# Optimization experiments

Measured on AMD Instinct MI355X. Metric: run time of the kernel, lower is better.

The kernel has to match this reference:

```python
import jax, jax.numpy as jnp
import numpy as np

D_MODEL = 1024
N_HEAD = 16
D_HEAD = D_MODEL // N_HEAD
N_EXPERTS = 8
TOP_K = 2
D_FF = 4096
EPS = 1e-6


def setup_inputs() -> dict:
    key = jax.random.key(0)
    ks = jax.random.split(key, 16)
    s = 0.02  # init scale
    d, dff, E = D_MODEL, D_FF, N_EXPERTS
    return {
        "dec": jax.random.normal(ks[0], (4, 1024, d), jnp.float32),
        "text_encoder": jax.random.normal(ks[1], (4, 512, d), jnp.float32),
        # self-attention projections
        "Wq1": jax.random.normal(ks[2], (d, d), jnp.float32) * s,
        "Wk1": jax.random.normal(ks[3], (d, d), jnp.float32) * s,
        "Wv1": jax.random.normal(ks[4], (d, d), jnp.float32) * s,
        "Wo1": jax.random.normal(ks[5], (d, d), jnp.float32) * s,
        # cross-attention projections
        "Wq2": jax.random.normal(ks[6], (d, d), jnp.float32) * s,
        "Wk2": jax.random.normal(ks[7], (d, d), jnp.float32) * s,
        "Wv2": jax.random.normal(ks[8], (d, d), jnp.float32) * s,
        "Wo2": jax.random.normal(ks[9], (d, d), jnp.float32) * s,
        # shared RMSNorm gain (module uses one norm instance three times)
        "g": jnp.ones((d,), jnp.float32),
        # MoE router + per-expert FFN weights
        "Wg": jax.random.normal(ks[10], (d, E), jnp.float32) * s,
        "W1": jax.random.normal(ks[11], (E, d, dff), jnp.float32) * s,
        "W2": jax.random.normal(ks[12], (E, dff, d), jnp.float32) * s,
    }


def rmsnorm(x, g):
    return x * jax.lax.rsqrt(jnp.mean(x * x, axis=-1, keepdims=True) + EPS) * g


def mha(q_in, k_in, v_in, Wq, Wk, Wv, Wo):
    B, Sq, _ = q_in.shape
    Sk = k_in.shape[1]
    q = (q_in @ Wq).reshape(B, Sq, N_HEAD, D_HEAD)
    k = (k_in @ Wk).reshape(B, Sk, N_HEAD, D_HEAD)
    v = (v_in @ Wv).reshape(B, Sk, N_HEAD, D_HEAD)
    scores = jnp.einsum("bqhd,bkhd->bhqk", q, k) / jnp.sqrt(jnp.asarray(D_HEAD, q.dtype))
    attn = jax.nn.softmax(scores, axis=-1)
    out = jnp.einsum("bhqk,bkhd->bqhd", attn, v).reshape(B, Sq, D_MODEL)
    return out @ Wo


def moe(x, Wg, W1, W2):
    # top-k softmax router, renormalized weights; dense per-expert FFN with combine
    probs = jax.nn.softmax(x @ Wg, axis=-1)              # [B,S,E]
    weights, indices = jax.lax.top_k(probs, TOP_K)        # [B,S,k]
    weights = weights / jnp.sum(weights, axis=-1, keepdims=True)
    # combine[t,e] = sum_k weights[t,k] * (indices[t,k]==e)
    combine = jnp.sum(
        jax.nn.one_hot(indices, N_EXPERTS, dtype=x.dtype) * weights[..., None], axis=-2
    )  # [B,S,E]
    out = jnp.zeros_like(x)
    for e in range(N_EXPERTS):  # fixed small expert loop
        h = jax.nn.relu(x @ W1[e]) @ W2[e]
        out = out + combine[..., e:e + 1] * h
    return weights, indices, out


def reference(dec, text_encoder, Wq1, Wk1, Wv1, Wo1, Wq2, Wk2, Wv2, Wo2, g, Wg, W1, W2):
    # self-attention + residual + RMSNorm (dropout p=0 -> identity)
    x = rmsnorm(mha(dec, dec, dec, Wq1, Wk1, Wv1, Wo1) + dec, g)
    # cross-attention + residual + RMSNorm
    x = rmsnorm(mha(x, text_encoder, text_encoder, Wq2, Wk2, Wv2, Wo2) + x, g)
    # MoE FFN + residual + RMSNorm
    weights, indices, y = moe(x, Wg, W1, W2)
    x = rmsnorm(y + x, g)
    return weights, indices, x
```

## Files before the change

### kernel.cpp

```cpp
#include <hip/hip_runtime.h>
#include <stdint.h>

#define D_    1024
#define BB    4
#define SDEC  1024
#define STXT  512
#define TDEC  4096
#define TTXT  2048
#define NH    16
#define DHD   64
#define NE    8
#define DFF   4096
#define NSLOT 8192
#define ND1   8192
#define ND2   4096
#define MOEGRID 1024

using u16 = unsigned short;
typedef __attribute__((ext_vector_type(8))) short bf16x8;
typedef __attribute__((ext_vector_type(4))) float f32x4;

__device__ __forceinline__ float bf2f(u16 h) {
    union { unsigned int u; float f; } x; x.u = ((unsigned int)h) << 16; return x.f;
}
__device__ __forceinline__ u16 f2bf(float f) {
    union { float f; unsigned int u; } x; x.f = f;
    unsigned int lsb = (x.u >> 16) & 1u;
    return (u16)((x.u + 0x7fffu + lsb) >> 16);
}

__device__ __forceinline__ void gld16(const u16* g, u16* l) {
    __builtin_amdgcn_global_load_lds((const __attribute__((address_space(1))) void*)g,
                                     (__attribute__((address_space(3))) void*)l,
                                     16, 0, 0);
}

constexpr int BM = 128, BK = 32;

template<int SPLIT, int EPI, int BROWS>
__global__ __launch_bounds__(256) void gemm_bt(
    const u16* __restrict__ AH, const u16* __restrict__ AL,
    const u16* __restrict__ BH, const u16* __restrict__ BL,
    float* __restrict__ Cf, u16* __restrict__ CH, u16* __restrict__ CL,
    int M, int N, int K, int lda, int ldb, int ldc,
    long strA, long strB, long strC)
{
    constexpr int WM = (BROWS == 64) ? 2 : 4;
    constexpr int ASZ = BM * BK, BSZ = BROWS * BK;
    __shared__ u16 smem[(SPLIT ? 2 : 1) * (ASZ + BSZ)];
    u16* sAH = smem;
    u16* sBH = smem + ASZ;
    u16* sAL = SPLIT ? smem + ASZ + BSZ : nullptr;
    u16* sBL = SPLIT ? smem + 2 * ASZ + BSZ : nullptr;

    const int z = blockIdx.z;
    const long zA = (long)z * strA, zB = (long)z * strB, zC = (long)z * strC;

    const int tileM = blockIdx.y * BM, tileN = blockIdx.x * BROWS;
    const int t = threadIdx.x;
    const int sr = t >> 2;
    const int sc = (t & 3) << 3;
    const u16* pA = AH + zA + (long)(tileM + sr) * lda + sc;
    const u16* pB = BH + zB + (long)(tileN + sr) * ldb + sc;
    const u16* pAl = nullptr; const u16* pBl = nullptr;
    if constexpr (SPLIT) {
        pAl = AL + zA + (long)(tileM + sr) * lda + sc;
        pBl = BL + zB + (long)(tileN + sr) * ldb + sc;
    }
    const long hA = 64L * lda, hB = 64L * ldb;

    const int lane = t & 63;
    const int wv = t >> 6;
    const int wr = (BROWS == 64) ? (wv << 5) : ((wv >> 1) << 6);
    const int wc = (BROWS == 64) ? 0 : ((wv & 1) << 6);
    const int fr = lane & 15, kg = lane >> 4;

    f32x4 acc[WM][4];
    const f32x4 vzero = {0.f, 0.f, 0.f, 0.f};
#pragma unroll
    for (int m = 0; m < WM; ++m)
#pragma unroll
        for (int n = 0; n < 4; ++n) acc[m][n] = vzero;

    for (int k0 = 0; k0 < K; k0 += BK) {
        gld16(pA + k0,      sAH + t * 8);
        gld16(pA + k0 + hA, sAH + 2048 + t * 8);
        gld16(pB + k0,      sBH + t * 8);
        if constexpr (BROWS == 128) gld16(pB + k0 + hB, sBH + 2048 + t * 8);
        if constexpr (SPLIT) {
            gld16(pAl + k0,      sAL + t * 8);
            gld16(pAl + k0 + hA, sAL + 2048 + t * 8);
            gld16(pBl + k0,      sBL + t * 8);
            if constexpr (BROWS == 128) gld16(pBl + k0 + hB, sBL + 2048 + t * 8);
        }
        __syncthreads();

        bf16x8 fa[WM], fb[4], fal[WM], fbl[4];
#pragma unroll
        for (int m = 0; m < WM; ++m) {
            fa[m] = *(const bf16x8*)&sAH[(wr + m * 16 + fr) * BK + (kg << 3)];
            if constexpr (SPLIT) fal[m] = *(const bf16x8*)&sAL[(wr + m * 16 + fr) * BK + (kg << 3)];
        }
#pragma unroll
        for (int n = 0; n < 4; ++n) {
            fb[n] = *(const bf16x8*)&sBH[(wc + n * 16 + fr) * BK + (kg << 3)];
            if constexpr (SPLIT) fbl[n] = *(const bf16x8*)&sBL[(wc + n * 16 + fr) * BK + (kg << 3)];
        }
#pragma unroll
        for (int m = 0; m < WM; ++m)
#pragma unroll
            for (int n = 0; n < 4; ++n) {
                acc[m][n] = __builtin_amdgcn_mfma_f32_16x16x32_bf16(fa[m], fb[n], acc[m][n], 0, 0, 0);
                if constexpr (SPLIT) {
                    acc[m][n] = __builtin_amdgcn_mfma_f32_16x16x32_bf16(fa[m],  fbl[n], acc[m][n], 0, 0, 0);
                    acc[m][n] = __builtin_amdgcn_mfma_f32_16x16x32_bf16(fal[m], fb[n],  acc[m][n], 0, 0, 0);
                }
            }
        __syncthreads();
    }

#pragma unroll
    for (int m = 0; m < WM; ++m) {
        const int r0 = tileM + wr + m * 16 + (kg << 2);
#pragma unroll
        for (int n = 0; n < 4; ++n) {
            const int col = tileN + wc + n * 16 + fr;
            if (col >= N) continue;
#pragma unroll
            for (int i = 0; i < 4; ++i) {
                const int r = r0 + i;
                if (r >= M) continue;
                const float v = acc[m][n][i];
                const long off = zC + (long)r * ldc + col;
                if constexpr (EPI == 0) {
                    Cf[off] = v;
                } else if constexpr (EPI == 1) {
                    const u16 h = f2bf(v);
                    CH[off] = h;
                    CL[off] = f2bf(v - bf2f(h));
                } else {
                    CH[off] = f2bf(fmaxf(v, 0.f));
                }
            }
        }
    }
}

template<int EPI>
__global__ __launch_bounds__(256, 4) void moe_gemm2(
    const u16* __restrict__ Ag, int lda,
    const u16* __restrict__ BTbase, int ldb, long btStride,
    float* __restrict__ Cf0, float* __restrict__ Cf1, u16* __restrict__ CH, int ldc,
    const int4* __restrict__ desc, int ndesc, int Kiter)
{
    __shared__ u16 smem[16384];
    const int t = threadIdx.x;
    const int lane = t & 63, wv = t >> 6;
    const int wr = (wv >> 1) << 6, wc = (wv & 1) << 6;
    const int fr = lane & 15, kg = lane >> 4;
    const int nks = Kiter >> 5;

    const int rS = t >> 2;
    const int cS = ((t & 3) ^ ((t >> 3) & 3)) << 3;

    int ldsA[4], ldsB[4];
#pragma unroll
    for (int m = 0; m < 4; ++m) {
        const int ra = wr + m * 16 + fr;
        ldsA[m] = ra * 32 + ((kg ^ ((ra >> 1) & 3)) << 3);
        const int rb = wc + m * 16 + fr;
        ldsB[m] = rb * 32 + ((kg ^ ((rb >> 1) & 3)) << 3);
    }

    for (int p = blockIdx.x; p < ndesc; p += MOEGRID) {
        const int4 d = desc[p];
        if (d.x < 0) continue;
        const int rowbase = d.x, colbase = d.y & 0xFFFF, e = d.y >> 16;
        const int kbase = d.z, s1 = d.w;
        const u16* paS = Ag + (long)(rowbase + rS) * lda + kbase + cS;
        const u16* pbS = BTbase + (long)e * btStride + (long)(colbase + rS) * ldb + kbase + cS;
        const long hA = 64L * lda, hB = 64L * ldb;

        f32x4 acc[4][4];
        const f32x4 vzero = {0.f, 0.f, 0.f, 0.f};
#pragma unroll
        for (int m = 0; m < 4; ++m)
#pragma unroll
            for (int n = 0; n < 4; ++n) acc[m][n] = vzero;

#define STG(ks, buf) { const long k0_ = (long)(ks) << 5; \
        u16* sA_ = smem + (buf) * 8192; \
        gld16(paS + k0_,      sA_ + t * 8); \
        gld16(paS + k0_ + hA, sA_ + 2048 + t * 8); \
        gld16(pbS + k0_,      sA_ + 4096 + t * 8); \
        gld16(pbS + k0_ + hB, sA_ + 6144 + t * 8); }

        STG(0, 0);
        asm volatile("s_waitcnt vmcnt(0)" ::: "memory");
        __builtin_amdgcn_s_barrier();

        for (int ks = 0; ks < nks; ++ks) {
            const int cur = ks & 1;
            if (ks + 1 < nks) STG(ks + 1, cur ^ 1);
            const u16* sA = smem + cur * 8192;
            const u16* sB = sA + 4096;
            bf16x8 fa[4], fb[4];
#pragma unroll
            for (int m = 0; m < 4; ++m) fa[m] = *(const bf16x8*)&sA[ldsA[m]];
#pragma unroll
            for (int n = 0; n < 4; ++n) fb[n] = *(const bf16x8*)&sB[ldsB[n]];
#pragma unroll
            for (int m = 0; m < 4; ++m)
#pragma unroll
                for (int n = 0; n < 4; ++n)
                    acc[m][n] = __builtin_amdgcn_mfma_f32_16x16x32_bf16(fa[m], fb[n], acc[m][n], 0, 0, 0);
            asm volatile("s_waitcnt vmcnt(0)" ::: "memory");
            __builtin_amdgcn_s_barrier();
        }
#undef STG

        float* __restrict__ C = (EPI == 0) ? ((kbase == 0) ? Cf0 : Cf1) : nullptr;
#pragma unroll
        for (int m = 0; m < 4; ++m) {
            const int r0 = rowbase + wr + m * 16 + (kg << 2);
#pragma unroll
            for (int n = 0; n < 4; ++n) {
                const int col = colbase + wc + n * 16 + fr;
#pragma unroll
                for (int i = 0; i < 4; ++i) {
                    const int r = r0 + i;
                    if (r >= s1) continue;
                    const float v = acc[m][n][i];
                    const long off = (long)r * ldc + col;
                    if constexpr (EPI == 0) C[off] = v;
                    else                    CH[off] = f2bf(fmaxf(v, 0.f));
                }
            }
        }
    }
}

__global__ __launch_bounds__(256) void split2k(const float* __restrict__ in,
                                               u16* __restrict__ oh, u16* __restrict__ ol, long n)
{
    long i = ((long)blockIdx.x * 256 + threadIdx.x) * 4;
    if (i >= n) return;
    float4 v = *(const float4*)(in + i);
    u16 h0 = f2bf(v.x), h1 = f2bf(v.y), h2 = f2bf(v.z), h3 = f2bf(v.w);
    uint2 oo;
    oo.x = (unsigned)h0 | ((unsigned)h1 << 16);
    oo.y = (unsigned)h2 | ((unsigned)h3 << 16);
    *(uint2*)(oh + i) = oo;
    if (ol) {
        u16 l0 = f2bf(v.x - bf2f(h0)), l1 = f2bf(v.y - bf2f(h1));
        u16 l2 = f2bf(v.z - bf2f(h2)), l3 = f2bf(v.w - bf2f(h3));
        uint2 ll;
        ll.x = (unsigned)l0 | ((unsigned)l1 << 16);
        ll.y = (unsigned)l2 | ((unsigned)l3 << 16);
        *(uint2*)(ol + i) = ll;
    }
}

__global__ __launch_bounds__(256) void transpose_split(
    const float* __restrict__ in, u16* __restrict__ oh, u16* __restrict__ ol,
    int R, int C, int ild, long ibs1, long ibs2, int nb2, int old_, long obs)
{
    __shared__ float tile[32][33];
    const int z = blockIdx.z;
    const float* ip = in + (long)(z / nb2) * ibs1 + (long)(z % nb2) * ibs2;
    u16* ohp = oh + (long)z * obs;
    u16* olp = ol ? ol + (long)z * obs : nullptr;
    const int c0 = blockIdx.x * 32, r0 = blockIdx.y * 32;
    const int tx = threadIdx.x & 31, ty = threadIdx.x >> 5;
    for (int i = ty; i < 32; i += 8) {
        int r = r0 + i, c = c0 + tx;
        tile[i][tx] = (r < R && c < C) ? ip[(long)r * ild + c] : 0.f;
    }
    __syncthreads();
    for (int i = ty; i < 32; i += 8) {
        int oc = c0 + i, orr = r0 + tx;
        if (oc < C && orr < R) {
            float v = tile[tx][i];
            u16 h = f2bf(v);
            ohp[(long)oc * old_ + orr] = h;
            if (olp) olp[(long)oc * old_ + orr] = f2bf(v - bf2f(h));
        }
    }
}

__global__ __launch_bounds__(256) void transpose_split_hl(
    const u16* __restrict__ inH, const u16* __restrict__ inL,
    u16* __restrict__ oh, u16* __restrict__ ol,
    int R, int C, int ild, long ibs1, long ibs2, int nb2, int old_, long obs)
{
    __shared__ float tile[32][33];
    const int z = blockIdx.z;
    const long base = (long)(z / nb2) * ibs1 + (long)(z % nb2) * ibs2;
    u16* ohp = oh + (long)z * obs;
    u16* olp = ol + (long)z * obs;
    const int c0 = blockIdx.x * 32, r0 = blockIdx.y * 32;
    const int tx = threadIdx.x & 31, ty = threadIdx.x >> 5;
    for (int i = ty; i < 32; i += 8) {
        int r = r0 + i, c = c0 + tx;
        float v = 0.f;
        if (r < R && c < C) {
            const long o = base + (long)r * ild + c;
            v = bf2f(inH[o]) + bf2f(inL[o]);
        }
        tile[i][tx] = v;
    }
    __syncthreads();
    for (int i = ty; i < 32; i += 8) {
        int oc = c0 + i, orr = r0 + tx;
        if (oc < C && orr < R) {
            float v = tile[tx][i];
            u16 h = f2bf(v);
            ohp[(long)oc * old_ + orr] = h;
            olp[(long)oc * old_ + orr] = f2bf(v - bf2f(h));
        }
    }
}

__global__ __launch_bounds__(256) void softmax_split(
    const float* __restrict__ s, u16* __restrict__ ph, u16* __restrict__ pl,
    int cols, float scale)
{
    const float* p = s + (long)blockIdx.x * cols;
    u16* php = ph + (long)blockIdx.x * cols;
    u16* plp = pl + (long)blockIdx.x * cols;
    const int t = threadIdx.x;
    float v[4];
    int vpt;
    if (cols == 1024) {
        vpt = 4;
        float4 x = ((const float4*)p)[t];
        v[0] = x.x * scale; v[1] = x.y * scale; v[2] = x.z * scale; v[3] = x.w * scale;
    } else {
        vpt = 2;
        float2 x = ((const float2*)p)[t];
        v[0] = x.x * scale; v[1] = x.y * scale; v[2] = -3.4e38f; v[3] = -3.4e38f;
    }
    float mx = fmaxf(fmaxf(v[0], v[1]), fmaxf(v[2], v[3]));
#pragma unroll
    for (int o = 32; o; o >>= 1) mx = fmaxf(mx, __shfl_xor(mx, o));
    __shared__ float sm[4];
    const int wv = t >> 6, ln = t & 63;
    if (ln == 0) sm[wv] = mx;
    __syncthreads();
    mx = fmaxf(fmaxf(sm[0], sm[1]), fmaxf(sm[2], sm[3]));
    float sum = 0.f;
    for (int i = 0; i < vpt; ++i) { v[i] = expf(v[i] - mx); sum += v[i]; }
#pragma unroll
    for (int o = 32; o; o >>= 1) sum += __shfl_xor(sum, o);
    __shared__ float ss[4];
    if (ln == 0) ss[wv] = sum;
    __syncthreads();
    sum = ss[0] + ss[1] + ss[2] + ss[3];
    const float inv = 1.f / sum;
    if (cols == 1024) {
        float q0 = v[0] * inv, q1 = v[1] * inv, q2 = v[2] * inv, q3 = v[3] * inv;
        u16 h0 = f2bf(q0), h1 = f2bf(q1), h2 = f2bf(q2), h3 = f2bf(q3);
        uint2 hh; hh.x = (unsigned)h0 | ((unsigned)h1 << 16); hh.y = (unsigned)h2 | ((unsigned)h3 << 16);
        ((uint2*)php)[t] = hh;
        u16 l0 = f2bf(q0 - bf2f(h0)), l1 = f2bf(q1 - bf2f(h1));
        u16 l2 = f2bf(q2 - bf2f(h2)), l3 = f2bf(q3 - bf2f(h3));
        uint2 ll; ll.x = (unsigned)l0 | ((unsigned)l1 << 16); ll.y = (unsigned)l2 | ((unsigned)l3 << 16);
        ((uint2*)plp)[t] = ll;
    } else {
        float q0 = v[0] * inv, q1 = v[1] * inv;
        u16 h0 = f2bf(q0), h1 = f2bf(q1);
        ((unsigned*)php)[t] = (unsigned)h0 | ((unsigned)h1 << 16);
        u16 l0 = f2bf(q0 - bf2f(h0)), l1 = f2bf(q1 - bf2f(h1));
        ((unsigned*)plp)[t] = (unsigned)l0 | ((unsigned)l1 << 16);
    }
}

__global__ __launch_bounds__(256) void add_rmsnorm(
    const float* __restrict__ a, const float* __restrict__ b, const float* __restrict__ g,
    float* __restrict__ xo, u16* __restrict__ xh, u16* __restrict__ xl)
{
    const long row = blockIdx.x;
    const int t = threadIdx.x;
    const float* pa = a + row * D_;
    const float* pb = b + row * D_;
    float v[4]; double ssq = 0.0;
#pragma unroll
    for (int i = 0; i < 4; ++i) {
        int c = t + (i << 8);
        v[i] = pa[c] + pb[c];
        ssq += (double)v[i] * v[i];
    }
#pragma unroll
    for (int o = 32; o; o >>= 1) ssq += __shfl_xor(ssq, o);
    __shared__ double sd[4];
    if ((t & 63) == 0) sd[t >> 6] = ssq;
    __syncthreads();
    ssq = sd[0] + sd[1] + sd[2] + sd[3];
    const float rs = (float)(1.0 / sqrt(ssq * (1.0 / 1024.0) + 1e-6));
#pragma unroll
    for (int i = 0; i < 4; ++i) {
        int c = t + (i << 8);
        float o = v[i] * rs * g[c];
        xo[row * D_ + c] = o;
        if (xh) {
            u16 h = f2bf(o);
            xh[row * D_ + c] = h;
            if (xl) xl[row * D_ + c] = f2bf(o - bf2f(h));
        }
    }
}

__global__ __launch_bounds__(256) void router_topk(
    const float* __restrict__ x2, const float* __restrict__ Wg,
    float* __restrict__ outw, float* __restrict__ outi,
    int* __restrict__ idx, float* __restrict__ tokw, int* __restrict__ counts, int T)
{
    const int wid = (int)((blockIdx.x * 256 + threadIdx.x) >> 6);
    const int lane = threadIdx.x & 63;
    if (wid >= T) return;
    float acc[NE];
#pragma unroll
    for (int e = 0; e < NE; ++e) acc[e] = 0.f;
    const float* xr = x2 + (long)wid * D_;
    for (int i = 0; i < 16; ++i) {
        float xv = xr[i * 64 + lane];
        const float* wr = Wg + (long)(i * 64 + lane) * NE;
#pragma unroll
        for (int e = 0; e < NE; ++e) acc[e] += xv * wr[e];
    }
#pragma unroll
    for (int e = 0; e < NE; ++e)
#pragma unroll
        for (int o = 32; o; o >>= 1) acc[e] += __shfl_xor(acc[e], o);
    if (lane == 0) {
        float m = acc[0];
#pragma unroll
        for (int e = 1; e < NE; ++e) m = fmaxf(m, acc[e]);
        float p[NE], s = 0.f;
#pragma unroll
        for (int e = 0; e < NE; ++e) { p[e] = expf(acc[e] - m); s += p[e]; }
        const float invs = 1.f / s;
#pragma unroll
        for (int e = 0; e < NE; ++e) p[e] *= invs;
        int e0 = 0;
#pragma unroll
        for (int e = 1; e < NE; ++e) if (p[e] > p[e0]) e0 = e;
        int e1 = (e0 == 0) ? 1 : 0;
#pragma unroll
        for (int e = 0; e < NE; ++e) if (e != e0 && e != e1 && p[e] > p[e1]) e1 = e;
        float w0 = p[e0], w1 = p[e1];
        const float sw = 1.f / (w0 + w1);
        w0 *= sw; w1 *= sw;
        outw[2 * wid] = w0;      outw[2 * wid + 1] = w1;
        outi[2 * wid] = (float)e0; outi[2 * wid + 1] = (float)e1;
        idx[2 * wid] = e0;       idx[2 * wid + 1] = e1;
        tokw[2 * wid] = w0;      tokw[2 * wid + 1] = w1;
        atomicAdd(&counts[e0], 1);
        atomicAdd(&counts[e1], 1);
    }
}

__global__ void scan_desc(const int* __restrict__ counts, int* __restrict__ cursor,
                          int4* __restrict__ d1, int4* __restrict__ d2)
{
    __shared__ int sseg[NE + 1];
    if (threadIdx.x == 0) {
        int a = 0;
        for (int e = 0; e < NE; ++e) { sseg[e] = a; cursor[e] = a; a += counts[e]; }
        sseg[NE] = a;
    }
    __syncthreads();
    const int e = threadIdx.x;
    if (e < NE) {
        const int s0 = sseg[e], s1 = sseg[e + 1];
        const int nyt = (s1 - s0 + 127) >> 7;
        for (int xt = 0; xt < 32; ++xt)
            for (int yt = 0; yt < nyt; ++yt)
                d1[e + 8 * (xt * nyt + yt)] =
                    make_int4(s0 + yt * 128, (xt * 128) | (e << 16), 0, s1);
        for (int kh = 0; kh < 2; ++kh)
            for (int xt = 0; xt < 8; ++xt)
                for (int yt = 0; yt < nyt; ++yt)
                    d2[e + 8 * ((kh * 8 + xt) * nyt + yt)] =
                        make_int4(s0 + yt * 128, (xt * 128) | (e << 16), kh * 2048, s1);
    }
}

__global__ __launch_bounds__(256) void scatter_slots(
    const int* __restrict__ idx, int* __restrict__ cursor,
    int* __restrict__ row_token, int* __restrict__ slot_of, int T)
{
    const int t = blockIdx.x * 256 + threadIdx.x;
    if (t >= T) return;
#pragma unroll
    for (int k = 0; k < 2; ++k) {
        const int e = idx[2 * t + k];
        const int pos = atomicAdd(&cursor[e], 1);
        row_token[pos] = t;
        slot_of[2 * t + k] = pos;
    }
}

__global__ __launch_bounds__(256) void gather_bf16(
    const float* __restrict__ x2, const int* __restrict__ row_token, u16* __restrict__ Xg)
{
    const int r = blockIdx.x;
    const int t = threadIdx.x;
    const float* src = x2 + (long)row_token[r] * D_ + t * 4;
    float4 v = *(const float4*)src;
    uint2 oo;
    oo.x = (unsigned)f2bf(v.x) | ((unsigned)f2bf(v.y) << 16);
    oo.y = (unsigned)f2bf(v.z) | ((unsigned)f2bf(v.w) << 16);
    *(uint2*)(Xg + (long)r * D_ + t * 4) = oo;
}

__global__ __launch_bounds__(256) void combine_rmsnorm(
    const float* __restrict__ Y0, const float* __restrict__ Y1,
    const int* __restrict__ slot_of, const float* __restrict__ tokw,
    const float* __restrict__ x2, const float* __restrict__ g, float* __restrict__ out)
{
    const long tr = blockIdx.x;
    const int t = threadIdx.x;
    const int s0 = slot_of[2 * tr], s1 = slot_of[2 * tr + 1];
    const float w0 = tokw[2 * tr], w1 = tokw[2 * tr + 1];
    const float* ya0 = Y0 + (long)s0 * D_;
    const float* yb0 = Y1 + (long)s0 * D_;
    const float* ya1 = Y0 + (long)s1 * D_;
    const float* yb1 = Y1 + (long)s1 * D_;
    const float* xr = x2 + tr * D_;
    float v[4]; double ssq = 0.0;
#pragma unroll
    for (int i = 0; i < 4; ++i) {
        int c = t + (i << 8);
        v[i] = w0 * (ya0[c] + yb0[c]) + w1 * (ya1[c] + yb1[c]) + xr[c];
        ssq += (double)v[i] * v[i];
    }
#pragma unroll
    for (int o = 32; o; o >>= 1) ssq += __shfl_xor(ssq, o);
    __shared__ double sd[4];
    if ((t & 63) == 0) sd[t >> 6] = ssq;
    __syncthreads();
    ssq = sd[0] + sd[1] + sd[2] + sd[3];
    const float rs = (float)(1.0 / sqrt(ssq * (1.0 / 1024.0) + 1e-6));
#pragma unroll
    for (int i = 0; i < 4; ++i) {
        int c = t + (i << 8);
        out[tr * D_ + c] = v[i] * rs * g[c];
    }
}

__global__ void sentinel(float* o) { o[0] = 12345.0f; }

extern "C" void kernel_launch(void* const* d_in, const int* in_sizes, int n_in,
                              void* d_out, int out_size, void* d_ws, size_t ws_size,
                              hipStream_t stream)
{
    const float* dec = (const float*)d_in[0];
    const float* te  = (const float*)d_in[1];
    const float* Win[8] = { (const float*)d_in[2], (const float*)d_in[3], (const float*)d_in[4],
                            (const float*)d_in[5], (const float*)d_in[6], (const float*)d_in[7],
                            (const float*)d_in[8], (const float*)d_in[9] };
    const float* g  = (const float*)d_in[10];
    const float* Wg = (const float*)d_in[11];
    const float* W1 = (const float*)d_in[12];
    const float* W2 = (const float*)d_in[13];
    float* outw = (float*)d_out;
    float* outi = outw + 2 * TDEC;
    float* outx = outw + 4 * TDEC;

    char* ws = (char*)d_ws;
    size_t off = 0;
    auto A = [&](size_t bytes) -> char* {
        char* p = ws + off;
        off += (bytes + 255) & ~(size_t)255;
        return p;
    };

    u16* decH = (u16*)A((size_t)TDEC * D_ * 2);
    u16* decL = (u16*)A((size_t)TDEC * D_ * 2);
    u16* teH  = (u16*)A((size_t)TTXT * D_ * 2);
    u16* teL  = (u16*)A((size_t)TTXT * D_ * 2);
    u16* wtHall = (u16*)A((size_t)8 * D_ * D_ * 2);
    u16* wtLall = (u16*)A((size_t)8 * D_ * D_ * 2);
    float* x1f = (float*)A((size_t)TDEC * D_ * 4);
    float* x2f = (float*)A((size_t)TDEC * D_ * 4);
    float* tokw = (float*)A(NSLOT * 4);
    int* idx    = (int*)A(NSLOT * 4);
    int* counts = (int*)A(256);
    int* cursor = (int*)A(256);
    int* row_token = (int*)A(NSLOT * 4);
    int* slot_of   = (int*)A(NSLOT * 4);
    int4* desc1 = (int4*)A((size_t)ND1 * 16);
    int4* desc2 = (int4*)A((size_t)ND2 * 16);

    const size_t Rbase = off;
    float* scores = (float*)A((size_t)NH * SDEC * SDEC * 4);
    u16* PH = (u16*)A((size_t)NH * SDEC * SDEC * 2);
    u16* PL = (u16*)A((size_t)NH * SDEC * SDEC * 2);
    u16* qkvH = (u16*)A((size_t)TDEC * 3 * D_ * 2);
    u16* qkvL = (u16*)A((size_t)TDEC * 3 * D_ * 2);
    u16* q2H  = (u16*)A((size_t)TDEC * D_ * 2);
    u16* q2L  = (u16*)A((size_t)TDEC * D_ * 2);
    u16* kv2H = (u16*)A((size_t)TTXT * 2 * D_ * 2);
    u16* kv2L = (u16*)A((size_t)TTXT * 2 * D_ * 2);
    u16* vTH = (u16*)A((size_t)TDEC * D_ * 2);
    u16* vTL = (u16*)A((size_t)TDEC * D_ * 2);
    u16* aoH = (u16*)A((size_t)TDEC * D_ * 2);
    u16* aoL = (u16*)A((size_t)TDEC * D_ * 2);
    u16* x1H = (u16*)A((size_t)TDEC * D_ * 2);
    u16* x1L = (u16*)A((size_t)TDEC * D_ * 2);
    float* of = (float*)A((size_t)TDEC * D_ * 4);
    const size_t attnEnd = off;

    off = Rbase;
    u16* W1T  = (u16*)A((size_t)NE * DFF * D_ * 2);
    u16* W2T  = (u16*)A((size_t)NE * D_ * DFF * 2);
    u16* Xg   = (u16*)A((size_t)(NSLOT + 256) * D_ * 2);
    u16* Hb   = (u16*)A((size_t)(NSLOT + 256) * DFF * 2);
    float* Yseg = (float*)A((size_t)NSLOT * D_ * 4);
    float* Ypart1 = (float*)W1T;
    const size_t needed = (off > attnEnd ? off : attnEnd);

    if (ws_size < needed) {
        sentinel<<<1, 1, 0, stream>>>(outw);
        return;
    }

    const dim3 blk(256);

    split2k<<<dim3((TDEC * D_) / 1024), blk, 0, stream>>>(dec, decH, decL, (long)TDEC * D_);
    split2k<<<dim3((TTXT * D_) / 1024), blk, 0, stream>>>(te, teH, teL, (long)TTXT * D_);
    for (int i = 0; i < 8; ++i)
        transpose_split<<<dim3(32, 32, 1), blk, 0, stream>>>(Win[i],
            wtHall + (size_t)i * D_ * D_, wtLall + (size_t)i * D_ * D_,
            D_, D_, D_, 0, 0, 1, D_, 0);

    gemm_bt<1, 1, 128><<<dim3(24, 32, 1), blk, 0, stream>>>(decH, decL, wtHall, wtLall,
        nullptr, qkvH, qkvL, TDEC, 3 * D_, D_, D_, D_, 3 * D_, 0, 0, 0);
    transpose_split_hl<<<dim3(2, 32, BB * NH), blk, 0, stream>>>(qkvH + 2 * D_, qkvL + 2 * D_,
        vTH, vTL, SDEC, DHD, 3 * D_, (long)SDEC * 3 * D_, DHD, NH, SDEC, (long)DHD * SDEC);

    for (int b = 0; b < BB; ++b) {
        const long qo3 = (long)b * SDEC * 3 * D_;
        const long qo  = (long)b * SDEC * D_;
        gemm_bt<1, 0, 128><<<dim3(8, 8, NH), blk, 0, stream>>>(
            qkvH + qo3, qkvL + qo3, qkvH + qo3 + D_, qkvL + qo3 + D_,
            scores, nullptr, nullptr, SDEC, SDEC, DHD, 3 * D_, 3 * D_, SDEC,
            DHD, DHD, (long)SDEC * SDEC);
        softmax_split<<<dim3(NH * SDEC), blk, 0, stream>>>(scores, PH, PL, SDEC, 0.125f);
        gemm_bt<1, 1, 64><<<dim3(1, 8, NH), blk, 0, stream>>>(PH, PL,
            vTH + (long)b * NH * DHD * SDEC, vTL + (long)b * NH * DHD * SDEC,
            nullptr, aoH + qo, aoL + qo, SDEC, DHD, SDEC, SDEC, SDEC, D_,
            (long)SDEC * SDEC, (long)DHD * SDEC, DHD);
    }
    gemm_bt<1, 0, 128><<<dim3(8, 32, 1), blk, 0, stream>>>(aoH, aoL,
        wtHall + (size_t)3 * D_ * D_, wtLall + (size_t)3 * D_ * D_,
        of, nullptr, nullptr, TDEC, D_, D_, D_, D_, D_, 0, 0, 0);
    add_rmsnorm<<<dim3(TDEC), blk, 0, stream>>>(of, dec, g, x1f, x1H, x1L);

    gemm_bt<1, 1, 128><<<dim3(8, 32, 1), blk, 0, stream>>>(x1H, x1L,
        wtHall + (size_t)4 * D_ * D_, wtLall + (size_t)4 * D_ * D_,
        nullptr, q2H, q2L, TDEC, D_, D_, D_, D_, D_, 0, 0, 0);
    gemm_bt<1, 1, 128><<<dim3(16, 16, 1), blk, 0, stream>>>(teH, teL,
        wtHall + (size_t)5 * D_ * D_, wtLall + (size_t)5 * D_ * D_,
        nullptr, kv2H, kv2L, TTXT, 2 * D_, D_, D_, D_, 2 * D_, 0, 0, 0);
    transpose_split_hl<<<dim3(2, 16, BB * NH), blk, 0, stream>>>(kv2H + D_, kv2L + D_,
        vTH, vTL, STXT, DHD, 2 * D_, (long)STXT * 2 * D_, DHD, NH, STXT, (long)DHD * STXT);

    for (int b = 0; b < BB; ++b) {
        const long qo  = (long)b * SDEC * D_;
        const long ko2 = (long)b * STXT * 2 * D_;
        gemm_bt<1, 0, 128><<<dim3(4, 8, NH), blk, 0, stream>>>(
            q2H + qo, q2L + qo, kv2H + ko2, kv2L + ko2,
            scores, nullptr, nullptr, SDEC, STXT, DHD, D_, 2 * D_, STXT,
            DHD, DHD, (long)SDEC * STXT);
        softmax_split<<<dim3(NH * SDEC), blk, 0, stream>>>(scores, PH, PL, STXT, 0.125f);
        gemm_bt<1, 1, 64><<<dim3(1, 8, NH), blk, 0, stream>>>(PH, PL,
            vTH + (long)b * NH * DHD * STXT, vTL + (long)b * NH * DHD * STXT,
            nullptr, aoH + qo, aoL + qo, SDEC, DHD, STXT, STXT, STXT, D_,
            (long)SDEC * STXT, (long)DHD * STXT, DHD);
    }
    gemm_bt<1, 0, 128><<<dim3(8, 32, 1), blk, 0, stream>>>(aoH, aoL,
        wtHall + (size_t)7 * D_ * D_, wtLall + (size_t)7 * D_ * D_,
        of, nullptr, nullptr, TDEC, D_, D_, D_, D_, D_, 0, 0, 0);
    add_rmsnorm<<<dim3(TDEC), blk, 0, stream>>>(of, x1f, g, x2f, nullptr, nullptr);

    hipMemsetAsync(counts, 0, 32, stream);
    hipMemsetAsync(desc1, 0xFF, (size_t)ND1 * 16, stream);
    hipMemsetAsync(desc2, 0xFF, (size_t)ND2 * 16, stream);
    router_topk<<<dim3(TDEC / 4), blk, 0, stream>>>(x2f, Wg, outw, outi, idx, tokw, counts, TDEC);
    scan_desc<<<1, 64, 0, stream>>>(counts, cursor, desc1, desc2);
    scatter_slots<<<dim3(TDEC / 256), blk, 0, stream>>>(idx, cursor, row_token, slot_of, TDEC);
    gather_bf16<<<dim3(NSLOT), blk, 0, stream>>>(x2f, row_token, Xg);

    transpose_split<<<dim3(DFF / 32, D_ / 32, NE), blk, 0, stream>>>(W1, W1T, nullptr,
        D_, DFF, DFF, (long)D_ * DFF, 0, 1, D_, (long)DFF * D_);
    transpose_split<<<dim3(D_ / 32, DFF / 32, NE), blk, 0, stream>>>(W2, W2T, nullptr,
        DFF, D_, D_, (long)D_ * DFF, 0, 1, DFF, (long)D_ * DFF);
    moe_gemm2<2><<<dim3(MOEGRID), blk, 0, stream>>>(Xg, D_, W1T, D_, (long)DFF * D_,
        nullptr, nullptr, Hb, DFF, desc1, ND1, 1024);
    moe_gemm2<0><<<dim3(MOEGRID), blk, 0, stream>>>(Hb, DFF, W2T, DFF, (long)D_ * DFF,
        Yseg, Ypart1, nullptr, D_, desc2, ND2, 2048);
    combine_rmsnorm<<<dim3(TDEC), blk, 0, stream>>>(Yseg, Ypart1, slot_of, tokw, x2f, g, outx);

    (void)in_sizes; (void)n_in; (void)out_size;
}
```

Baseline: 1.453 ms.

## Split-K the P·V attention GEMM and triple-buffer the MoE GEMM pipeline

The P·V product, which launched only 128 blocks per batch, is replaced by a split-K kernel over four K quarters (512 blocks) that writes fp32 partials, followed by a combine kernel that sums them and emits hi/lo bf16 output. The aim is to fill the GPU better on this narrow GEMM, at the cost of extra partial-buffer traffic and one more launch. Separately, the MoE GEMM goes from double to triple buffering with partial vmcnt waits, sched barriers and setprio around the MFMAs. This raises LDS use and lowers the occupancy bound from 4 to 3.

```diff
diff --git a/kernel.cpp b/kernel.cpp
--- a/kernel.cpp
+++ b/kernel.cpp
@@ -146,14 +146,124 @@
     }
 }
 
+__global__ __launch_bounds__(256) void pv_gemm(
+    const u16* __restrict__ PHp, const u16* __restrict__ PLp,
+    const u16* __restrict__ VTH, const u16* __restrict__ VTL,
+    float* __restrict__ Op, int Skv)
+{
+    __shared__ u16 smem[12288];
+    u16* sAH = smem;
+    u16* sAL = smem + 4096;
+    u16* sBH = smem + 8192;
+    u16* sBL = smem + 10240;
+
+    const int kq = blockIdx.x;
+    const int tileM = blockIdx.y * 128;
+    const int z = blockIdx.z;
+    const int kbase = kq * (Skv >> 2);
+    const int nks = Skv >> 7;
+
+    const int t = threadIdx.x;
+    const int sr = t >> 2, sc = (t & 3) << 3;
+    const u16* pA  = PHp + (long)z * 1024 * Skv + (long)(tileM + sr) * Skv + kbase + sc;
+    const u16* pAl = PLp + (long)z * 1024 * Skv + (long)(tileM + sr) * Skv + kbase + sc;
+    const u16* pB  = VTH + (long)z * 64 * Skv + (long)sr * Skv + kbase + sc;
+    const u16* pBl = VTL + (long)z * 64 * Skv + (long)sr * Skv + kbase + sc;
+    const long hA = 64L * Skv;
+
+    const int lane = t & 63, wv = t >> 6;
+    const int wr = wv << 5;
+    const int fr = lane & 15, kg = lane >> 4;
+
+    f32x4 acc[2][4];
+    const f32x4 vzero = {0.f, 0.f, 0.f, 0.f};
+#pragma unroll
+    for (int m = 0; m < 2; ++m)
+#pragma unroll
+        for (int n = 0; n < 4; ++n) acc[m][n] = vzero;
+
+    for (int ks = 0; ks < nks; ++ks) {
+        const long k0 = (long)ks << 5;
+        gld16(pA + k0,       sAH + t * 8);
+        gld16(pA + k0 + hA,  sAH + 2048 + t * 8);
+        gld16(pAl + k0,      sAL + t * 8);
+        gld16(pAl + k0 + hA, sAL + 2048 + t * 8);
+        gld16(pB + k0,       sBH + t * 8);
+        gld16(pBl + k0,      sBL + t * 8);
+        __syncthreads();
+        bf16x8 fa[2], fb[4], fal[2], fbl[4];
+#pragma unroll
+        for (int m = 0; m < 2; ++m) {
+            fa[m]  = *(const bf16x8*)&sAH[(wr + m * 16 + fr) * 32 + (kg << 3)];
+            fal[m] = *(const bf16x8*)&sAL[(wr + m * 16 + fr) * 32 + (kg << 3)];
+        }
+#pragma unroll
+        for (int n = 0; n < 4; ++n) {
+            fb[n]  = *(const bf16x8*)&sBH[(n * 16 + fr) * 32 + (kg << 3)];
+            fbl[n] = *(const bf16x8*)&sBL[(n * 16 + fr) * 32 + (kg << 3)];
+        }
+#pragma unroll
+        for (int m = 0; m < 2; ++m)
+#pragma unroll
+            for (int n = 0; n < 4; ++n) {
+                acc[m][n] = __builtin_amdgcn_mfma_f32_16x16x32_bf16(fa[m],  fb[n],  acc[m][n], 0, 0, 0);
+                acc[m][n] = __builtin_amdgcn_mfma_f32_16x16x32_bf16(fa[m],  fbl[n], acc[m][n], 0, 0, 0);
+                acc[m][n] = __builtin_amdgcn_mfma_f32_16x16x32_bf16(fal[m], fb[n],  acc[m][n], 0, 0, 0);
+            }
+        __syncthreads();
+    }
+
+    const long base = ((long)kq * NH + z) * 65536;
+#pragma unroll
+    for (int m = 0; m < 2; ++m) {
+        const int r0 = tileM + wr + m * 16 + (kg << 2);
+#pragma unroll
+        for (int n = 0; n < 4; ++n) {
+            const int col = n * 16 + fr;
+#pragma unroll
+            for (int i = 0; i < 4; ++i)
+                Op[base + (long)(r0 + i) * 64 + col] = acc[m][n][i];
+        }
+    }
+}
+
+__global__ __launch_bounds__(256) void pv_combine(
+    const float* __restrict__ Op, u16* __restrict__ aoH, u16* __restrict__ aoL)
+{
+    const long i = ((long)blockIdx.x * 256 + threadIdx.x) * 4;
+    const int z = (int)(i >> 16);
+    const int rem = (int)(i & 65535);
+    const int r = rem >> 6, c = rem & 63;
+    float4 v = *(const float4*)(Op + i);
+    const float4 v1 = *(const float4*)(Op + 1048576 + i);
+    const float4 v2 = *(const float4*)(Op + 2097152 + i);
+    const float4 v3 = *(const float4*)(Op + 3145728 + i);
+    v.x += v1.x + v2.x + v3.x;
+    v.y += v1.y + v2.y + v3.y;
+    v.z += v1.z + v2.z + v3.z;
+    v.w += v1.w + v2.w + v3.w;
+    const long dst = (long)r * D_ + z * 64 + c;
+    u16 h0 = f2bf(v.x), h1 = f2bf(v.y), h2 = f2bf(v.z), h3 = f2bf(v.w);
+    uint2 hh;
+    hh.x = (unsigned)h0 | ((unsigned)h1 << 16);
+    hh.y = (unsigned)h2 | ((unsigned)h3 << 16);
+    *(uint2*)(aoH + dst) = hh;
+    u16 l0 = f2bf(v.x - bf2f(h0)), l1 = f2bf(v.y - bf2f(h1));
+    u16 l2 = f2bf(v.z - bf2f(h2)), l3 = f2bf(v.w - bf2f(h3));
+    uint2 ll;
+    ll.x = (unsigned)l0 | ((unsigned)l1 << 16);
+    ll.y = (unsigned)l2 | ((unsigned)l3 << 16);
+    *(uint2*)(aoL + dst) = ll;
+}
+
 template<int EPI>
-__global__ __launch_bounds__(256, 4) void moe_gemm2(
+__global__ __launch_bounds__(256, 3) void moe_gemm2(
     const u16* __restrict__ Ag, int lda,
     const u16* __restrict__ BTbase, int ldb, long btStride,
     float* __restrict__ Cf0, float* __restrict__ Cf1, u16* __restrict__ CH, int ldc,
     const int4* __restrict__ desc, int ndesc, int Kiter)
 {
-    __shared__ u16 smem[16384];
+    __shared__ u16 smem[24576];
     const int t = threadIdx.x;
     const int lane = t & 63, wv = t >> 6;
     const int wr = (wv >> 1) << 6, wc = (wv & 1) << 6;
@@ -188,34 +298,38 @@
 #pragma unroll
             for (int n = 0; n < 4; ++n) acc[m][n] = vzero;
 
-#define STG(ks, buf) { const long k0_ = (long)(ks) << 5; \
-        u16* sA_ = smem + (buf) * 8192; \
-        gld16(paS + k0_,      sA_ + t * 8); \
-        gld16(paS + k0_ + hA, sA_ + 2048 + t * 8); \
-        gld16(pbS + k0_,      sA_ + 4096 + t * 8); \
-        gld16(pbS + k0_ + hB, sA_ + 6144 + t * 8); }
-
-        STG(0, 0);
-        asm volatile("s_waitcnt vmcnt(0)" ::: "memory");
+#define STG(ks) { const int s_ = (ks) % 3; const long k0_ = (long)(ks) << 5; \
+        u16* b_ = smem + s_ * 8192; \
+        gld16(paS + k0_,      b_ + t * 8); \
+        gld16(paS + k0_ + hA, b_ + 2048 + t * 8); \
+        gld16(pbS + k0_,      b_ + 4096 + t * 8); \
+        gld16(pbS + k0_ + hB, b_ + 6144 + t * 8); }
+
+        STG(0); STG(1);
+        asm volatile("s_waitcnt vmcnt(4)" ::: "memory");
         __builtin_amdgcn_s_barrier();
+        __builtin_amdgcn_sched_barrier(0);
 
         for (int ks = 0; ks < nks; ++ks) {
-            const int cur = ks & 1;
-            if (ks + 1 < nks) STG(ks + 1, cur ^ 1);
-            const u16* sA = smem + cur * 8192;
+            if (ks + 2 < nks) STG(ks + 2);
+            const u16* sA = smem + (ks % 3) * 8192;
             const u16* sB = sA + 4096;
             bf16x8 fa[4], fb[4];
 #pragma unroll
             for (int m = 0; m < 4; ++m) fa[m] = *(const bf16x8*)&sA[ldsA[m]];
 #pragma unroll
             for (int n = 0; n < 4; ++n) fb[n] = *(const bf16x8*)&sB[ldsB[n]];
+            __builtin_amdgcn_s_setprio(1);
 #pragma unroll
             for (int m = 0; m < 4; ++m)
 #pragma unroll
                 for (int n = 0; n < 4; ++n)
                     acc[m][n] = __builtin_amdgcn_mfma_f32_16x16x32_bf16(fa[m], fb[n], acc[m][n], 0, 0, 0);
-            asm volatile("s_waitcnt vmcnt(0)" ::: "memory");
+            __builtin_amdgcn_s_setprio(0);
+            if (ks + 2 < nks) { asm volatile("s_waitcnt vmcnt(4)" ::: "memory"); }
+            else              { asm volatile("s_waitcnt vmcnt(0)" ::: "memory"); }
             __builtin_amdgcn_s_barrier();
+            __builtin_amdgcn_sched_barrier(0);
         }
 #undef STG
 
@@ -610,6 +724,7 @@
     u16* x1H = (u16*)A((size_t)TDEC * D_ * 2);
     u16* x1L = (u16*)A((size_t)TDEC * D_ * 2);
     float* of = (float*)A((size_t)TDEC * D_ * 4);
+    float* Opart = (float*)A((size_t)4 * NH * SDEC * DHD * 4);
     const size_t attnEnd = off;
 
     off = Rbase;
@@ -648,10 +763,9 @@
             scores, nullptr, nullptr, SDEC, SDEC, DHD, 3 * D_, 3 * D_, SDEC,
             DHD, DHD, (long)SDEC * SDEC);
         softmax_split<<<dim3(NH * SDEC), blk, 0, stream>>>(scores, PH, PL, SDEC, 0.125f);
-        gemm_bt<1, 1, 64><<<dim3(1, 8, NH), blk, 0, stream>>>(PH, PL,
-            vTH + (long)b * NH * DHD * SDEC, vTL + (long)b * NH * DHD * SDEC,
-            nullptr, aoH + qo, aoL + qo, SDEC, DHD, SDEC, SDEC, SDEC, D_,
-            (long)SDEC * SDEC, (long)DHD * SDEC, DHD);
+        pv_gemm<<<dim3(4, 8, NH), blk, 0, stream>>>(PH, PL,
+            vTH + (long)b * NH * DHD * SDEC, vTL + (long)b * NH * DHD * SDEC, Opart, SDEC);
+        pv_combine<<<dim3(1024), blk, 0, stream>>>(Opart, aoH + qo, aoL + qo);
     }
     gemm_bt<1, 0, 128><<<dim3(8, 32, 1), blk, 0, stream>>>(aoH, aoL,
         wtHall + (size_t)3 * D_ * D_, wtLall + (size_t)3 * D_ * D_,
@@ -675,10 +789,9 @@
             scores, nullptr, nullptr, SDEC, STXT, DHD, D_, 2 * D_, STXT,
             DHD, DHD, (long)SDEC * STXT);
         softmax_split<<<dim3(NH * SDEC), blk, 0, stream>>>(scores, PH, PL, STXT, 0.125f);
-        gemm_bt<1, 1, 64><<<dim3(1, 8, NH), blk, 0, stream>>>(PH, PL,
-            vTH + (long)b * NH * DHD * STXT, vTL + (long)b * NH * DHD * STXT,
-            nullptr, aoH + qo, aoL + qo, SDEC, DHD, STXT, STXT, STXT, D_,
-            (long)SDEC * STXT, (long)DHD * STXT, DHD);
+        pv_gemm<<<dim3(4, 8, NH), blk, 0, stream>>>(PH, PL,
+            vTH + (long)b * NH * DHD * STXT, vTL + (long)b * NH * DHD * STXT, Opart, STXT);
+        pv_combine<<<dim3(1024), blk, 0, stream>>>(Opart, aoH + qo, aoL + qo);
     }
     gemm_bt<1, 0, 128><<<dim3(8, 32, 1), blk, 0, stream>>>(aoH, aoL,
         wtHall + (size_t)7 * D_ * D_, wtLall + (size_t)7 * D_ * D_,
```

Result: faster. 1.401 ms (-3.6%).
